# Performance work log

Hardware: AMD Instinct MI355X
Metric: run time of the kernel (lower is better)

The kernel has to match this reference:

```python
import jax, jax.numpy as jnp
import numpy as np

N, M, F_IN, F_OUT, B = 8192, 4096, 256, 128, 2048
NEG = -9e15
EPS = 1e-5


def leaky(x, slope=0.2):
    return jnp.where(x > 0, x, slope * x)


def batchnorm(x, gamma, beta):
    # BatchNorm1d training-mode semantics: biased batch stats over dim 0
    m = x.mean(axis=0)
    v = jnp.var(x, axis=0)
    return (x - m) * jax.lax.rsqrt(v + EPS) * gamma + beta


def setup_inputs() -> dict:
    key = jax.random.key(0)
    ks = jax.random.split(key, 12)
    inp = {}
    inp["Sinput"] = jax.random.normal(ks[0], (N, F_IN), dtype=jnp.float32)
    inp["Rinput"] = jax.random.normal(ks[1], (M, F_IN), dtype=jnp.float32)
    inp["inter_adj"] = jax.random.randint(ks[2], (N, M), 0, 2).astype(jnp.int32)
    inp["city_adj"] = jax.random.randint(ks[3], (N, N), 0, 2).astype(jnp.int32)
    inp["province_adj"] = jax.random.randint(ks[4], (N, N), 0, 2).astype(jnp.int32)
    inp["source_index"] = jax.random.randint(ks[5], (B,), 0, N).astype(jnp.int32)
    s_w = 1.414 * np.sqrt(6.0 / (F_IN + F_OUT))  # xavier_uniform gain=1.414
    s_a = 1.414 * np.sqrt(6.0 / (2 * F_OUT + 1))
    inp["W1"] = jax.random.uniform(ks[6], (F_IN, F_OUT), jnp.float32, -s_w, s_w)
    inp["W2"] = jax.random.uniform(ks[7], (F_IN, F_OUT), jnp.float32, -s_w, s_w)
    inp["a"] = jax.random.uniform(ks[8], (2 * F_OUT, 1), jnp.float32, -s_a, s_a)
    inp["a3"] = jax.random.uniform(ks[9], (2 * F_OUT, 1), jnp.float32, -s_a, s_a)
    inp["a4"] = jax.random.uniform(ks[10], (2 * F_OUT, 1), jnp.float32, -s_a, s_a)
    inp["bn1_gamma"] = jnp.ones((F_OUT,), jnp.float32)
    inp["bn1_beta"] = jnp.zeros((F_OUT,), jnp.float32)
    inp["bn2_gamma"] = jnp.ones((F_OUT,), jnp.float32)
    inp["bn2_beta"] = jnp.zeros((F_OUT,), jnp.float32)
    return inp


def reference(Sinput, Rinput, inter_adj, city_adj, province_adj, source_index,
              W1, W2, a, a3, a4, bn1_gamma, bn1_beta, bn2_gamma, bn2_beta):
    F = W1.shape[1]
    h1 = Rinput @ W1            # [M, F]
    h2 = Sinput @ W2            # [N, F]
    # Decomposed GAT score: cat([h1[m], h2[n]]) @ a == h1[m]@a[:F] + h2[n]@a[F:]
    e12 = leaky((h2 @ a[F:, 0])[:, None] + (h1 @ a[:F, 0])[None, :])  # [N, M]
    att_inter = jax.nn.softmax(jnp.where(inter_adj > 0, e12, NEG), axis=1)
    h2_ = h2[source_index]      # [B, F]
    # cat([h2_, h2_]) @ a3 -> h2_ @ (a3[:F] + a3[F:]), constant along N axis
    s3 = leaky(h2_ @ (a3[:F, 0] + a3[F:, 0]))  # [B]
    s4 = leaky(h2_ @ (a4[:F, 0] + a4[F:, 0]))  # [B]
    Nn = Sinput.shape[0]
    e3 = jnp.broadcast_to(s3[:, None], (s3.shape[0], Nn))
    e4 = jnp.broadcast_to(s4[:, None], (s4.shape[0], Nn))
    att3 = jax.nn.softmax(jnp.where(city_adj[source_index] > 0, e3, NEG), axis=1)
    att4 = jax.nn.softmax(jnp.where(province_adj[source_index] > 0, e4, NEG), axis=1)
    InterRC = att_inter @ h1                    # [N, F]
    IntraNC = att3.T @ h2_ + att4.T @ h2_       # [N, F]
    v_output = leaky(batchnorm(att_inter.T @ h2, bn1_gamma, bn1_beta))  # [M, F]
    u_output = leaky(batchnorm(InterRC + IntraNC, bn2_gamma, bn2_beta))  # [N, F]
    h_prime = u_output @ v_output.T             # [N, M]
    return jax.nn.elu(h_prime)
```

## Files before the change

kernel.cpp:

```cpp
#include <hip/hip_runtime.h>
#include <stdint.h>

#define N_ 8192
#define M_ 4096
#define FIN_ 256
#define F_ 128
#define B_ 2048

typedef __attribute__((ext_vector_type(8))) short vs8;
typedef __attribute__((ext_vector_type(8))) __bf16 vb8;
typedef __attribute__((ext_vector_type(4))) float vf4;

union ABu { vs8 s; vb8 b; };

__device__ __forceinline__ vf4 mfma16(const ABu& a, const ABu& b, vf4 c) {
    return __builtin_amdgcn_mfma_f32_16x16x32_bf16(a.b, b.b, c, 0, 0, 0);
}
__device__ __forceinline__ unsigned short f2b(float x) {
    union { float f; unsigned u; } v; v.f = x;
    unsigned r = v.u + 0x7fffu + ((v.u >> 16) & 1u);
    return (unsigned short)(r >> 16);
}
__device__ __forceinline__ float lrelu(float x) { return x > 0.f ? x : 0.2f * x; }

__device__ __forceinline__ void glds16(const unsigned short* g, void* l) {
    __builtin_amdgcn_global_load_lds((const __attribute__((address_space(1))) unsigned int*)g,
                                     (__attribute__((address_space(3))) unsigned int*)l, 16, 0, 0);
}

__global__ void k_prep(const float* __restrict__ W1, const float* __restrict__ W2,
                       unsigned short* __restrict__ W1T, unsigned short* __restrict__ W2T,
                       float4* __restrict__ Z, int nz4) {
    int id = blockIdx.x * 256 + threadIdx.x;
    if (id < 65536) {
        const float* W = (id < 32768) ? W1 : W2;
        unsigned short* WT = (id < 32768) ? W1T : W2T;
        int o = id & 32767;
        int f = o >> 8, k = o & 255;
        WT[o] = f2b(W[k * F_ + f]);
    } else {
        int z = id - 65536;
        if (z < nz4) Z[z] = make_float4(0.f, 0.f, 0.f, 0.f);
    }
}

__global__ __launch_bounds__(256) void k_hgemmF(const float* __restrict__ Rin, const float* __restrict__ Sin,
                                                const unsigned short* __restrict__ W1T,
                                                const unsigned short* __restrict__ W2T,
                                                const float* __restrict__ a,
                                                float* __restrict__ h2,
                                                unsigned short* __restrict__ h1P, unsigned short* __restrict__ h2P,
                                                float* __restrict__ s1, float* __restrict__ s2) {
    __shared__ unsigned short tb[16][136];
    __shared__ float sred[4][16];
    int t = threadIdx.x;
    int w = t >> 6, l = t & 63, lr = l & 15, lg = l >> 4;
    int gr = blockIdx.x * 16;
    const float* X; const unsigned short* WT; unsigned short* HP; float* sout; const float* av;
    int row0; bool isH2;
    if (gr < M_) { X = Rin; WT = W1T; HP = h1P; sout = s1; av = a;      row0 = gr;      isH2 = false; }
    else         { X = Sin; WT = W2T; HP = h2P; sout = s2; av = a + F_; row0 = gr - M_; isH2 = true;  }
    int fbase = w * 32;
    vf4 acc[2] = {};
    const float* xp = X + (size_t)(row0 + lr) * FIN_ + lg * 8;
#pragma unroll
    for (int kk = 0; kk < FIN_; kk += 32) {
        float4 xa = *(const float4*)(xp + kk);
        float4 xb = *(const float4*)(xp + kk + 4);
        ABu af;
        af.s[0] = (short)f2b(xa.x); af.s[1] = (short)f2b(xa.y);
        af.s[2] = (short)f2b(xa.z); af.s[3] = (short)f2b(xa.w);
        af.s[4] = (short)f2b(xb.x); af.s[5] = (short)f2b(xb.y);
        af.s[6] = (short)f2b(xb.z); af.s[7] = (short)f2b(xb.w);
#pragma unroll
        for (int q = 0; q < 2; ++q) {
            ABu bf; bf.s = *(const vs8*)(WT + (fbase + q * 16 + lr) * FIN_ + kk + lg * 8);
            acc[q] = mfma16(af, bf, acc[q]);
        }
    }
    if (isH2) {
#pragma unroll
        for (int q = 0; q < 2; ++q)
#pragma unroll
            for (int r = 0; r < 4; ++r)
                h2[(size_t)(row0 + lg * 4 + r) * F_ + fbase + q * 16 + lr] = acc[q][r];
    }
#pragma unroll
    for (int q = 0; q < 2; ++q)
#pragma unroll
        for (int r = 0; r < 4; ++r)
            tb[lg * 4 + r][fbase + q * 16 + lr] = f2b(acc[q][r]);
    float a0 = av[fbase + lr], a1 = av[fbase + 16 + lr];
    float tv[4];
#pragma unroll
    for (int r = 0; r < 4; ++r) tv[r] = acc[0][r] * a0 + acc[1][r] * a1;
#pragma unroll
    for (int off = 1; off < 16; off <<= 1)
#pragma unroll
        for (int r = 0; r < 4; ++r) tv[r] += __shfl_xor(tv[r], off, 64);
    if ((l & 15) == 0)
#pragma unroll
        for (int r = 0; r < 4; ++r) sred[w][lg * 4 + r] = tv[r];
    __syncthreads();
    {
        int f = t >> 1, half = t & 1;
        vs8 o;
#pragma unroll
        for (int j = 0; j < 8; ++j) o[j] = (short)tb[half * 8 + j][f];
        *(vs8*)(HP + ((size_t)(row0 >> 5) * 128 + f) * 32 + (row0 & 16) + half * 8) = o;
    }
    if (t < 16) {
        float s = sred[0][t] + sred[1][t] + sred[2][t] + sred[3][t];
        sout[row0 + t] = s;
    }
}

__global__ __launch_bounds__(256) void k_adjgather(const int* __restrict__ inter, const float* __restrict__ s1,
                                                   const float* __restrict__ s2, unsigned short* __restrict__ bm,
                                                   float* __restrict__ rowmax, float* __restrict__ rowinv,
                                                   const int* __restrict__ city, const int* __restrict__ prov,
                                                   const int* __restrict__ src,
                                                   uint32_t* __restrict__ BMtc, uint32_t* __restrict__ BMtp,
                                                   float* __restrict__ w3, float* __restrict__ w4,
                                                   const float* __restrict__ h2, unsigned short* __restrict__ h2wP) {
    __shared__ float wred[8];
    int t = threadIdx.x;
    int wv = t >> 6, ln = t & 63;
    if (blockIdx.x < N_) {
        int n = blockIdx.x;
        const int* rp = inter + (size_t)n * M_ + t * 16;
        float sv[16]; unsigned mask = 0;
#pragma unroll
        for (int c = 0; c < 4; ++c) {
            int4 v = *(const int4*)(rp + c * 4);
            if (v.x > 0) mask |= 1u << (c * 4 + 0);
            if (v.y > 0) mask |= 1u << (c * 4 + 1);
            if (v.z > 0) mask |= 1u << (c * 4 + 2);
            if (v.w > 0) mask |= 1u << (c * 4 + 3);
            float4 s = *(const float4*)(s1 + t * 16 + c * 4);
            sv[c * 4 + 0] = s.x; sv[c * 4 + 1] = s.y; sv[c * 4 + 2] = s.z; sv[c * 4 + 3] = s.w;
        }
        bm[(size_t)n * 256 + t] = (unsigned short)(mask & 0xffffu);
        float mx = -3.0e38f;
#pragma unroll
        for (int j = 0; j < 16; ++j) if (mask & (1u << j)) mx = fmaxf(mx, sv[j]);
        for (int off = 32; off > 0; off >>= 1) mx = fmaxf(mx, __shfl_down(mx, off, 64));
        if (ln == 0) wred[wv] = mx;
        __syncthreads();
        float s1mx = fmaxf(fmaxf(wred[0], wred[1]), fmaxf(wred[2], wred[3]));
        float s2n = s2[n];
        float rmx = lrelu(s2n + s1mx);
        float sum = 0.f;
#pragma unroll
        for (int j = 0; j < 16; ++j) if (mask & (1u << j)) sum += __expf(lrelu(s2n + sv[j]) - rmx);
        for (int off = 32; off > 0; off >>= 1) sum += __shfl_down(sum, off, 64);
        if (ln == 0) wred[4 + wv] = sum;
        __syncthreads();
        if (t == 0) {
            float tot = wred[4] + wred[5] + wred[6] + wred[7];
            bool any = s1mx > -2.9e38f;
            rowmax[n] = any ? rmx : 0.f;
            rowinv[n] = (any && tot > 0.f) ? 1.0f / tot : 0.f;
        }
    } else if (blockIdx.x < N_ + 2 * B_) {
        int bb = blockIdx.x - N_;
        int b = bb & (B_ - 1);
        bool isC = bb < B_;
        const int* adj = isC ? city : prov;
        uint32_t* BM = isC ? BMtc : BMtp;
        float* wout = isC ? w3 : w4;
        const int* rowp = adj + (size_t)src[b] * N_;
        int cnt = 0;
#pragma unroll 4
        for (int i = 0; i < N_ / 256; ++i) {
            int v = rowp[i * 256 + t];
            unsigned long long bal = __ballot(v > 0);
            cnt += (v > 0);
            if (ln == 0) {
                int widx = i * 8 + wv * 2;
                BM[(size_t)widx * B_ + b] = (uint32_t)bal;
                BM[(size_t)(widx + 1) * B_ + b] = (uint32_t)(bal >> 32);
            }
        }
        float fc = (float)cnt;
        for (int off = 32; off > 0; off >>= 1) fc += __shfl_down(fc, off, 64);
        if (ln == 0) wred[wv] = fc;
        __syncthreads();
        if (t == 0) {
            float tot = wred[0] + wred[1] + wred[2] + wred[3];
            wout[b] = tot > 0.f ? 1.0f / tot : 0.f;
        }
    } else {
        int bblk = blockIdx.x - (N_ + 2 * B_);
        int f = t & 127, halfb = t >> 7;
        vs8 o0, o1;
#pragma unroll
        for (int i = 0; i < 8; ++i) {
            int b0 = bblk * 32 + halfb * 16 + i;
            o0[i] = (short)f2b(h2[(size_t)src[b0] * F_ + f]);
            int b1 = b0 + 8;
            o1[i] = (short)f2b(h2[(size_t)src[b1] * F_ + f]);
        }
        unsigned short* dst = h2wP + ((size_t)bblk * 128 + f) * 32 + halfb * 16;
        *(vs8*)dst = o0;
        *(vs8*)(dst + 8) = o1;
    }
}

__global__ __launch_bounds__(256) void k_attmat2(const unsigned char* __restrict__ bm8,
                                                 const float* __restrict__ s1, const float* __restrict__ s2,
                                                 const float* __restrict__ rowmax, const float* __restrict__ rowinv,
                                                 unsigned short* __restrict__ attP,
                                                 unsigned short* __restrict__ attT) {
    __shared__ unsigned short tile[64][33];
    int bx = blockIdx.x;
    int mt = bx & 63, nt = bx >> 6;
    int nb = nt * 32, mb = mt * 64;
    int t = threadIdx.x;
    int mo = t & 7, nl = t >> 3;
    int n = nb + nl;
    int m = mb + mo * 8;
    unsigned bits = bm8[(size_t)n * 512 + (m >> 3)];
    float s2n = s2[n], rmx = rowmax[n], rin = rowinv[n];
    float4 sa = *(const float4*)(s1 + m);
    float4 sb = *(const float4*)(s1 + m + 4);
    float sv[8] = {sa.x, sa.y, sa.z, sa.w, sb.x, sb.y, sb.z, sb.w};
    vs8 o;
#pragma unroll
    for (int j = 0; j < 8; ++j) {
        float v = (bits & (1u << j)) ? __expf(lrelu(s2n + sv[j]) - rmx) * rin : 0.f;
        o[j] = (short)f2b(v);
        tile[mo * 8 + j][nl] = (unsigned short)o[j];
    }
    *(vs8*)(attP + ((size_t)(m >> 5) * N_ + n) * 32 + (m & 31)) = o;
    __syncthreads();
    int mr = t >> 2, sg = t & 3;
    vs8 ot;
#pragma unroll
    for (int j = 0; j < 8; ++j) ot[j] = (short)tile[mr][sg * 8 + j];
    *(vs8*)(attT + ((size_t)nt * M_ + mb + mr) * 32 + sg * 8) = ot;
}

__global__ __launch_bounds__(256) void k_gemmABC(const unsigned short* __restrict__ attP,
                                                 const unsigned short* __restrict__ attT,
                                                 const unsigned short* __restrict__ h1P,
                                                 const unsigned short* __restrict__ h2P,
                                                 const uint32_t* __restrict__ BMtc, const uint32_t* __restrict__ BMtp,
                                                 const float* __restrict__ w3, const float* __restrict__ w4,
                                                 const unsigned short* __restrict__ h2wP,
                                                 float* __restrict__ uP, float* __restrict__ vP) {
    __shared__ __align__(16) unsigned short smem[24576];
    int t = threadIdx.x;
    int w = t >> 6, l = t & 63;
    int lr = l & 15, lg = l >> 4;
    int bx = blockIdx.x;
    if (bx < 1024) {
        bool isA = bx < 512;
        int i = isA ? bx : bx - 512;
        int x, y, rowsK;
        const unsigned short* Asrc; const unsigned short* Bsrc; float* Out;
        if (isA) { x = i & 127; y = i >> 7; Asrc = attP; Bsrc = h1P;
                   Out = uP + (size_t)y * N_ * F_; rowsK = N_; }
        else     { x = i & 63;  y = i >> 6; Asrc = attT; Bsrc = h2P;
                   Out = vP + (size_t)y * M_ * F_; rowsK = M_; }
        int kbase = y * 32;
        int rb0b = x * 64;
        int rh = (w & 1) * 32;
        int fb = (w >> 1) * 64;
        int ch0 = w * 6;
        auto stage = [&](int step, int curb) {
#pragma unroll
            for (int ii = 0; ii < 6; ++ii) {
                int c = ch0 + ii;
                const unsigned short* g; int loff;
                if (c < 8) {
                    int kb = c >> 2;
                    g = Asrc + (size_t)(kbase + 2 * step + kb) * rowsK * 32 + rb0b * 32
                        + (c & 3) * 512 + l * 8;
                    loff = curb * 24576 + kb * 4096 + (c & 3) * 1024;
                } else {
                    int c2 = c - 8;
                    int kb = c2 >> 3;
                    g = Bsrc + (size_t)(kbase + 2 * step + kb) * 4096 + (c2 & 7) * 512 + l * 8;
                    loff = curb * 24576 + 8192 + kb * 8192 + (c2 & 7) * 1024;
                }
                glds16(g, (char*)smem + loff);
            }
        };
        vf4 acc[2][4] = {};
        stage(0, 0);
        __syncthreads();
        int cur = 0;
        for (int step = 0; step < 16; ++step) {
            if (step < 15) stage(step + 1, cur ^ 1);
            const char* base = (const char*)smem + cur * 24576;
#pragma unroll
            for (int kb = 0; kb < 2; ++kb) {
                ABu a0, a1, b0, b1, b2, b3;
                a0.s = *(const vs8*)(base + kb * 4096 + (rh + lr) * 64 + lg * 16);
                a1.s = *(const vs8*)(base + kb * 4096 + (rh + 16 + lr) * 64 + lg * 16);
                b0.s = *(const vs8*)(base + 8192 + kb * 8192 + (fb + lr) * 64 + lg * 16);
                b1.s = *(const vs8*)(base + 8192 + kb * 8192 + (fb + 16 + lr) * 64 + lg * 16);
                b2.s = *(const vs8*)(base + 8192 + kb * 8192 + (fb + 32 + lr) * 64 + lg * 16);
                b3.s = *(const vs8*)(base + 8192 + kb * 8192 + (fb + 48 + lr) * 64 + lg * 16);
                acc[0][0] = mfma16(a0, b0, acc[0][0]);
                acc[1][0] = mfma16(a1, b0, acc[1][0]);
                acc[0][1] = mfma16(a0, b1, acc[0][1]);
                acc[1][1] = mfma16(a1, b1, acc[1][1]);
                acc[0][2] = mfma16(a0, b2, acc[0][2]);
                acc[1][2] = mfma16(a1, b2, acc[1][2]);
                acc[0][3] = mfma16(a0, b3, acc[0][3]);
                acc[1][3] = mfma16(a1, b3, acc[1][3]);
            }
            __syncthreads();
            cur ^= 1;
        }
#pragma unroll
        for (int s = 0; s < 2; ++s)
#pragma unroll
            for (int q = 0; q < 4; ++q)
#pragma unroll
                for (int r = 0; r < 4; ++r)
                    Out[(size_t)(rb0b + rh + s * 16 + lg * 4 + r) * F_ + fb + q * 16 + lr] = acc[s][q][r];
    } else {
        int i = bx - 1024;
        int xc = i & 127, yc = i >> 7;
        int nb0 = xc * 64 + (w & 1) * 32;
        int fb = (w >> 1) * 64;
        int wi = nb0 >> 5;
        const uint32_t* bc = BMtc + (size_t)wi * B_;
        const uint32_t* bp = BMtp + (size_t)wi * B_;
        vf4 acc[2][4] = {};
        int b0s = yc * (B_ / 4);
        for (int b0 = b0s; b0 < b0s + B_ / 4; b0 += 32) {
            int bb = b0 + lg * 8;
            uint4 c0 = *(const uint4*)(bc + bb);
            uint4 c1 = *(const uint4*)(bc + bb + 4);
            uint4 p0 = *(const uint4*)(bp + bb);
            uint4 p1 = *(const uint4*)(bp + bb + 4);
            float4 wa = *(const float4*)(w3 + bb);
            float4 wb = *(const float4*)(w3 + bb + 4);
            float4 wc = *(const float4*)(w4 + bb);
            float4 wd = *(const float4*)(w4 + bb + 4);
            const unsigned short* hb = h2wP + (size_t)(b0 >> 5) * 128 * 32;
            ABu bf0, bf1, bf2, bf3;
            bf0.s = *(const vs8*)(hb + (size_t)(fb + lr) * 32 + lg * 8);
            bf1.s = *(const vs8*)(hb + (size_t)(fb + 16 + lr) * 32 + lg * 8);
            bf2.s = *(const vs8*)(hb + (size_t)(fb + 32 + lr) * 32 + lg * 8);
            bf3.s = *(const vs8*)(hb + (size_t)(fb + 48 + lr) * 32 + lg * 8);
            uint32_t cw[8] = {c0.x, c0.y, c0.z, c0.w, c1.x, c1.y, c1.z, c1.w};
            uint32_t pw[8] = {p0.x, p0.y, p0.z, p0.w, p1.x, p1.y, p1.z, p1.w};
            float w3v[8] = {wa.x, wa.y, wa.z, wa.w, wb.x, wb.y, wb.z, wb.w};
            float w4v[8] = {wc.x, wc.y, wc.z, wc.w, wd.x, wd.y, wd.z, wd.w};
            ABu af0, af1;
#pragma unroll
            for (int j = 0; j < 8; ++j) {
                float v0 = (((cw[j] >> lr) & 1u) ? w3v[j] : 0.f) + (((pw[j] >> lr) & 1u) ? w4v[j] : 0.f);
                float v1 = (((cw[j] >> (16 + lr)) & 1u) ? w3v[j] : 0.f) + (((pw[j] >> (16 + lr)) & 1u) ? w4v[j] : 0.f);
                af0.s[j] = (short)f2b(v0);
                af1.s[j] = (short)f2b(v1);
            }
            acc[0][0] = mfma16(af0, bf0, acc[0][0]);
            acc[1][0] = mfma16(af1, bf0, acc[1][0]);
            acc[0][1] = mfma16(af0, bf1, acc[0][1]);
            acc[1][1] = mfma16(af1, bf1, acc[1][1]);
            acc[0][2] = mfma16(af0, bf2, acc[0][2]);
            acc[1][2] = mfma16(af1, bf2, acc[1][2]);
            acc[0][3] = mfma16(af0, bf3, acc[0][3]);
            acc[1][3] = mfma16(af1, bf3, acc[1][3]);
        }
        float* Out = uP + (size_t)(4 + yc) * N_ * F_;
#pragma unroll
        for (int s = 0; s < 2; ++s)
#pragma unroll
            for (int q = 0; q < 4; ++q)
#pragma unroll
                for (int r = 0; r < 4; ++r)
                    Out[(size_t)(nb0 + s * 16 + lg * 4 + r) * F_ + fb + q * 16 + lr] = acc[s][q][r];
    }
}

__global__ __launch_bounds__(256) void k_bnreduce(const float* __restrict__ vP, const float* __restrict__ uP,
                                                  float* __restrict__ v_in, float* __restrict__ u_in,
                                                  float* __restrict__ stats) {
    __shared__ float r1[256], r2[256];
    int bx = blockIdx.x;
    const float* P; float* O; int R, nb_; size_t stride; float* sum; float* sq;
    if (bx < 256) { P = vP; O = v_in; R = M_; nb_ = 256; stride = (size_t)M_ * F_;
                    sum = stats; sq = stats + 128; }
    else          { P = uP; O = u_in; R = N_; nb_ = 512; stride = (size_t)N_ * F_;
                    sum = stats + 256; sq = stats + 384; bx -= 256; }
    int f = threadIdx.x & 127;
    int half = threadIdx.x >> 7;
    float s = 0.f, s2v = 0.f;
    for (int r = bx * 2 + half; r < R; r += nb_ * 2) {
        float v = 0.f;
#pragma unroll
        for (int y = 0; y < 8; ++y) v += P[(size_t)y * stride + (size_t)r * F_ + f];
        O[(size_t)r * F_ + f] = v;
        s += v; s2v += v * v;
    }
    r1[threadIdx.x] = s; r2[threadIdx.x] = s2v;
    __syncthreads();
    if (half == 0) {
        atomicAdd(&sum[f], r1[f] + r1[f + 128]);
        atomicAdd(&sq[f], r2[f] + r2[f + 128]);
    }
}

__global__ __launch_bounds__(256) void k_bnapplyF(const float* __restrict__ v_in, const float* __restrict__ u_in,
                                                  const float* __restrict__ stats,
                                                  const float* __restrict__ g1, const float* __restrict__ b1,
                                                  const float* __restrict__ g2, const float* __restrict__ b2,
                                                  unsigned short* __restrict__ v_outb, unsigned short* __restrict__ u_outb) {
    __shared__ float sc[256], sh[256];
    int t = threadIdx.x;
    {
        int which = t >> 7, f = t & 127;
        const float* sum = stats + which * 256;
        const float* sq = sum + 128;
        const float* g = which ? g2 : g1;
        const float* be = which ? b2 : b1;
        float R = which ? (float)N_ : (float)M_;
        float mean = sum[f] / R;
        float var = sq[f] / R - mean * mean;
        float s = g[f] * rsqrtf(var + 1e-5f);
        sc[t] = s; sh[t] = be[f] - mean * s;
    }
    __syncthreads();
    int id4 = blockIdx.x * 256 + t;
    int idx = id4 * 4;
    int which = idx >= M_ * F_;
    int rel = which ? idx - M_ * F_ : idx;
    const float* P = which ? u_in : v_in;
    unsigned short* Q = which ? u_outb : v_outb;
    int f0 = (rel & 127) + which * 128;
    float4 p = *(const float4*)(P + rel);
    ushort4 o;
    o.x = f2b(lrelu(p.x * sc[f0 + 0] + sh[f0 + 0]));
    o.y = f2b(lrelu(p.y * sc[f0 + 1] + sh[f0 + 1]));
    o.z = f2b(lrelu(p.z * sc[f0 + 2] + sh[f0 + 2]));
    o.w = f2b(lrelu(p.w * sc[f0 + 3] + sh[f0 + 3]));
    *(ushort4*)(Q + rel) = o;
}

__global__ __launch_bounds__(256) void k_gemmD(const unsigned short* __restrict__ U,
                                               const unsigned short* __restrict__ V,
                                               float* __restrict__ out) {
    int w = threadIdx.x >> 6, l = threadIdx.x & 63;
    int lr = l & 15, lg = l >> 4;
    int nb = blockIdx.x * 64 + w * 16;
    int mb = blockIdx.y * 64;
    vf4 acc[4] = {};
#pragma unroll
    for (int k0 = 0; k0 < F_; k0 += 32) {
        ABu af; af.s = *(const vs8*)(U + (size_t)(nb + lr) * F_ + k0 + lg * 8);
#pragma unroll
        for (int q = 0; q < 4; ++q) {
            ABu bf; bf.s = *(const vs8*)(V + (size_t)(mb + q * 16 + lr) * F_ + k0 + lg * 8);
            acc[q] = mfma16(af, bf, acc[q]);
        }
    }
#pragma unroll
    for (int q = 0; q < 4; ++q)
#pragma unroll
        for (int r = 0; r < 4; ++r) {
            int row = nb + lg * 4 + r;
            int col = mb + q * 16 + lr;
            float x = acc[q][r];
            out[(size_t)row * M_ + col] = x > 0.f ? x : __expf(x) - 1.f;
        }
}

extern "C" void kernel_launch(void* const* d_in, const int* in_sizes, int n_in,
                              void* d_out, int out_size, void* d_ws, size_t ws_size,
                              hipStream_t stream) {
    const float* Sinput = (const float*)d_in[0];
    const float* Rinput = (const float*)d_in[1];
    const int* inter_adj = (const int*)d_in[2];
    const int* city_adj = (const int*)d_in[3];
    const int* prov_adj = (const int*)d_in[4];
    const int* src = (const int*)d_in[5];
    const float* W1 = (const float*)d_in[6];
    const float* W2 = (const float*)d_in[7];
    const float* a = (const float*)d_in[8];
    const float* g1 = (const float*)d_in[11];
    const float* b1 = (const float*)d_in[12];
    const float* g2 = (const float*)d_in[13];
    const float* b2 = (const float*)d_in[14];
    float* out = (float*)d_out;

    char* ws = (char*)d_ws;
    size_t o = 0;
    auto take = [&](size_t bytes) { char* p = ws + o; o += (bytes + 255) & ~(size_t)255; return p; };
    float* stats = (float*)take(512 * 4);
    size_t zero_bytes = o;
    float* u_in = (float*)take((size_t)N_ * F_ * 4);
    float* v_in = (float*)take((size_t)M_ * F_ * 4);
    float* uP = (float*)take((size_t)8 * N_ * F_ * 4);
    float* vP = (float*)take((size_t)8 * M_ * F_ * 4);
    float* h2 = (float*)take((size_t)N_ * F_ * 4);
    unsigned short* h1P = (unsigned short*)take((size_t)(M_ / 32) * 128 * 32 * 2);
    unsigned short* h2P = (unsigned short*)take((size_t)(N_ / 32) * 128 * 32 * 2);
    unsigned short* W1T = (unsigned short*)take((size_t)F_ * FIN_ * 2);
    unsigned short* W2T = (unsigned short*)take((size_t)F_ * FIN_ * 2);
    float* s1 = (float*)take(M_ * 4);
    float* s2 = (float*)take(N_ * 4);
    float* rowmax = (float*)take(N_ * 4);
    float* rowinv = (float*)take(N_ * 4);
    float* w3 = (float*)take(B_ * 4);
    float* w4 = (float*)take(B_ * 4);
    unsigned short* h2wP = (unsigned short*)take((size_t)(B_ / 32) * 128 * 32 * 2);
    unsigned short* u_outb = (unsigned short*)take((size_t)N_ * F_ * 2);
    unsigned short* v_outb = (unsigned short*)take((size_t)M_ * F_ * 2);
    uint32_t* BMtc = (uint32_t*)take((size_t)256 * B_ * 4);
    uint32_t* BMtp = (uint32_t*)take((size_t)256 * B_ * 4);
    unsigned short* bm = (unsigned short*)take((size_t)N_ * 256 * 2);
    unsigned short* attP = (unsigned short*)take((size_t)N_ * M_ * 2);
    unsigned short* attT = (unsigned short*)take((size_t)N_ * M_ * 2);
    (void)ws_size; (void)in_sizes; (void)n_in; (void)out_size;

    int nz4 = (int)(zero_bytes / 16);
    int zblocks = (nz4 + 255) / 256;
    k_prep<<<256 + zblocks, 256, 0, stream>>>(W1, W2, W1T, W2T, (float4*)d_ws, nz4);
    k_hgemmF<<<(M_ + N_) / 16, 256, 0, stream>>>(Rinput, Sinput, W1T, W2T, a, h2, h1P, h2P, s1, s2);
    k_adjgather<<<N_ + 2 * B_ + B_ / 32, 256, 0, stream>>>(inter_adj, s1, s2, bm, rowmax, rowinv,
                                                           city_adj, prov_adj, src, BMtc, BMtp, w3, w4,
                                                           h2, h2wP);
    k_attmat2<<<16384, 256, 0, stream>>>((const unsigned char*)bm, s1, s2, rowmax, rowinv, attP, attT);
    k_gemmABC<<<1536, 256, 0, stream>>>(attP, attT, h1P, h2P, BMtc, BMtp, w3, w4, h2wP, uP, vP);
    k_bnreduce<<<768, 256, 0, stream>>>(vP, uP, v_in, u_in, stats);
    k_bnapplyF<<<(M_ + N_) * F_ / 4 / 256, 256, 0, stream>>>(v_in, u_in, stats, g1, b1, g2, b2, v_outb, u_outb);
    k_gemmD<<<dim3(N_ / 64, M_ / 64), 256, 0, stream>>>(u_outb, v_outb, out);
}
```

Baseline: 327.0 us.

## Enlarge att GEMM tiles to 128x128 and rebalance split-K partial buffers

The attention GEMMs (att@h1 and att^T@h2) now use 128-row by 128-feature tiles, with each wave computing a 64x64 sub-tile (4x4 MFMA accumulators) instead of 32x64. This doubles operand reuse from shared memory and halves A-tile reloads. The att@h1 split-K changes to 8 slices of 16 steps, so the intra-city partials move to slots 8-11 and the u partial buffer grows to 12 slices. The bnreduce kernel sums 12 partials for u, which adds extra memory traffic and register pressure in exchange for fewer, larger GEMM blocks.

```diff
diff --git a/kernel.cpp b/kernel.cpp
--- a/kernel.cpp
+++ b/kernel.cpp
@@ -249,81 +249,63 @@
                                                  const float* __restrict__ w3, const float* __restrict__ w4,
                                                  const unsigned short* __restrict__ h2wP,
                                                  float* __restrict__ uP, float* __restrict__ vP) {
-    __shared__ __align__(16) unsigned short smem[24576];
+    __shared__ __align__(16) unsigned short smem[16384];
     int t = threadIdx.x;
     int w = t >> 6, l = t & 63;
     int lr = l & 15, lg = l >> 4;
     int bx = blockIdx.x;
-    if (bx < 1024) {
+    if (bx < 768) {
         bool isA = bx < 512;
         int i = isA ? bx : bx - 512;
-        int x, y, rowsK;
+        int x, y, ns, kbase, rowsK;
         const unsigned short* Asrc; const unsigned short* Bsrc; float* Out;
-        if (isA) { x = i & 127; y = i >> 7; Asrc = attP; Bsrc = h1P;
-                   Out = uP + (size_t)y * N_ * F_; rowsK = N_; }
-        else     { x = i & 63;  y = i >> 6; Asrc = attT; Bsrc = h2P;
-                   Out = vP + (size_t)y * M_ * F_; rowsK = M_; }
-        int kbase = y * 32;
-        int rb0b = x * 64;
-        int rh = (w & 1) * 32;
-        int fb = (w >> 1) * 64;
-        int ch0 = w * 6;
-        auto stage = [&](int step, int curb) {
-#pragma unroll
-            for (int ii = 0; ii < 6; ++ii) {
-                int c = ch0 + ii;
+        if (isA) { x = i & 63; y = i >> 6; ns = 16; kbase = y * 16; rowsK = N_;
+                   Asrc = attP; Bsrc = h1P; Out = uP + (size_t)y * N_ * F_; }
+        else     { x = i & 31; y = i >> 5; ns = 32; kbase = y * 32; rowsK = M_;
+                   Asrc = attT; Bsrc = h2P; Out = vP + (size_t)y * M_ * F_; }
+        int rb0 = x * 128;
+        int rq = (w >> 1) * 64;
+        int cb = (w & 1) * 64;
+        auto stage = [&](int kb, int buf) {
+#pragma unroll
+            for (int ii = 0; ii < 4; ++ii) {
+                int c = w * 4 + ii;
                 const unsigned short* g; int loff;
-                if (c < 8) {
-                    int kb = c >> 2;
-                    g = Asrc + (size_t)(kbase + 2 * step + kb) * rowsK * 32 + rb0b * 32
-                        + (c & 3) * 512 + l * 8;
-                    loff = curb * 24576 + kb * 4096 + (c & 3) * 1024;
-                } else {
-                    int c2 = c - 8;
-                    int kb = c2 >> 3;
-                    g = Bsrc + (size_t)(kbase + 2 * step + kb) * 4096 + (c2 & 7) * 512 + l * 8;
-                    loff = curb * 24576 + 8192 + kb * 8192 + (c2 & 7) * 1024;
-                }
-                glds16(g, (char*)smem + loff);
+                if (c < 8) { g = Asrc + ((size_t)kb * rowsK + rb0) * 32 + c * 512 + l * 8;
+                             loff = buf * 8192 + c * 512; }
+                else       { g = Bsrc + (size_t)kb * 4096 + (c - 8) * 512 + l * 8;
+                             loff = buf * 8192 + 4096 + (c - 8) * 512; }
+                glds16(g, smem + loff);
             }
         };
-        vf4 acc[2][4] = {};
-        stage(0, 0);
+        vf4 acc[4][4] = {};
+        stage(kbase, 0);
         __syncthreads();
         int cur = 0;
-        for (int step = 0; step < 16; ++step) {
-            if (step < 15) stage(step + 1, cur ^ 1);
-            const char* base = (const char*)smem + cur * 24576;
-#pragma unroll
-            for (int kb = 0; kb < 2; ++kb) {
-                ABu a0, a1, b0, b1, b2, b3;
-                a0.s = *(const vs8*)(base + kb * 4096 + (rh + lr) * 64 + lg * 16);
-                a1.s = *(const vs8*)(base + kb * 4096 + (rh + 16 + lr) * 64 + lg * 16);
-                b0.s = *(const vs8*)(base + 8192 + kb * 8192 + (fb + lr) * 64 + lg * 16);
-                b1.s = *(const vs8*)(base + 8192 + kb * 8192 + (fb + 16 + lr) * 64 + lg * 16);
-                b2.s = *(const vs8*)(base + 8192 + kb * 8192 + (fb + 32 + lr) * 64 + lg * 16);
-                b3.s = *(const vs8*)(base + 8192 + kb * 8192 + (fb + 48 + lr) * 64 + lg * 16);
-                acc[0][0] = mfma16(a0, b0, acc[0][0]);
-                acc[1][0] = mfma16(a1, b0, acc[1][0]);
-                acc[0][1] = mfma16(a0, b1, acc[0][1]);
-                acc[1][1] = mfma16(a1, b1, acc[1][1]);
-                acc[0][2] = mfma16(a0, b2, acc[0][2]);
-                acc[1][2] = mfma16(a1, b2, acc[1][2]);
-                acc[0][3] = mfma16(a0, b3, acc[0][3]);
-                acc[1][3] = mfma16(a1, b3, acc[1][3]);
-            }
+        for (int step = 0; step < ns; ++step) {
+            if (step + 1 < ns) stage(kbase + step + 1, cur ^ 1);
+            const unsigned short* base = smem + cur * 8192;
+            ABu a[4], b[4];
+#pragma unroll
+            for (int s = 0; s < 4; ++s) a[s].s = *(const vs8*)(base + (rq + s * 16 + lr) * 32 + lg * 8);
+#pragma unroll
+            for (int q = 0; q < 4; ++q) b[q].s = *(const vs8*)(base + 4096 + (cb + q * 16 + lr) * 32 + lg * 8);
+#pragma unroll
+            for (int s = 0; s < 4; ++s)
+#pragma unroll
+                for (int q = 0; q < 4; ++q) acc[s][q] = mfma16(a[s], b[q], acc[s][q]);
             __syncthreads();
             cur ^= 1;
         }
 #pragma unroll
-        for (int s = 0; s < 2; ++s)
+        for (int s = 0; s < 4; ++s)
 #pragma unroll
             for (int q = 0; q < 4; ++q)
 #pragma unroll
                 for (int r = 0; r < 4; ++r)
-                    Out[(size_t)(rb0b + rh + s * 16 + lg * 4 + r) * F_ + fb + q * 16 + lr] = acc[s][q][r];
+                    Out[(size_t)(rb0 + rq + s * 16 + lg * 4 + r) * F_ + cb + q * 16 + lr] = acc[s][q][r];
     } else {
-        int i = bx - 1024;
+        int i = bx - 768;
         int xc = i & 127, yc = i >> 7;
         int nb0 = xc * 64 + (w & 1) * 32;
         int fb = (w >> 1) * 64;
@@ -369,7 +351,7 @@
             acc[0][3] = mfma16(af0, bf3, acc[0][3]);
             acc[1][3] = mfma16(af1, bf3, acc[1][3]);
         }
-        float* Out = uP + (size_t)(4 + yc) * N_ * F_;
+        float* Out = uP + (size_t)(8 + yc) * N_ * F_;
 #pragma unroll
         for (int s = 0; s < 2; ++s)
 #pragma unroll
@@ -385,26 +367,40 @@
                                                   float* __restrict__ stats) {
     __shared__ float r1[256], r2[256];
     int bx = blockIdx.x;
-    const float* P; float* O; int R, nb_; size_t stride; float* sum; float* sq;
-    if (bx < 256) { P = vP; O = v_in; R = M_; nb_ = 256; stride = (size_t)M_ * F_;
-                    sum = stats; sq = stats + 128; }
-    else          { P = uP; O = u_in; R = N_; nb_ = 512; stride = (size_t)N_ * F_;
-                    sum = stats + 256; sq = stats + 384; bx -= 256; }
     int f = threadIdx.x & 127;
     int half = threadIdx.x >> 7;
     float s = 0.f, s2v = 0.f;
-    for (int r = bx * 2 + half; r < R; r += nb_ * 2) {
-        float v = 0.f;
-#pragma unroll
-        for (int y = 0; y < 8; ++y) v += P[(size_t)y * stride + (size_t)r * F_ + f];
-        O[(size_t)r * F_ + f] = v;
-        s += v; s2v += v * v;
-    }
-    r1[threadIdx.x] = s; r2[threadIdx.x] = s2v;
-    __syncthreads();
-    if (half == 0) {
-        atomicAdd(&sum[f], r1[f] + r1[f + 128]);
-        atomicAdd(&sq[f], r2[f] + r2[f + 128]);
+    if (bx < 256) {
+        size_t stride = (size_t)M_ * F_;
+        for (int r = bx * 2 + half; r < M_; r += 512) {
+            float v = 0.f;
+#pragma unroll
+            for (int y = 0; y < 8; ++y) v += vP[(size_t)y * stride + (size_t)r * F_ + f];
+            v_in[(size_t)r * F_ + f] = v;
+            s += v; s2v += v * v;
+        }
+        r1[threadIdx.x] = s; r2[threadIdx.x] = s2v;
+        __syncthreads();
+        if (half == 0) {
+            atomicAdd(&stats[f], r1[f] + r1[f + 128]);
+            atomicAdd(&stats[128 + f], r2[f] + r2[f + 128]);
+        }
+    } else {
+        int b = bx - 256;
+        size_t stride = (size_t)N_ * F_;
+        for (int r = b * 2 + half; r < N_; r += 1024) {
+            float v = 0.f;
+#pragma unroll
+            for (int y = 0; y < 12; ++y) v += uP[(size_t)y * stride + (size_t)r * F_ + f];
+            u_in[(size_t)r * F_ + f] = v;
+            s += v; s2v += v * v;
+        }
+        r1[threadIdx.x] = s; r2[threadIdx.x] = s2v;
+        __syncthreads();
+        if (half == 0) {
+            atomicAdd(&stats[256 + f], r1[f] + r1[f + 128]);
+            atomicAdd(&stats[384 + f], r2[f] + r2[f + 128]);
+        }
     }
 }
 
@@ -497,7 +493,7 @@
     size_t zero_bytes = o;
     float* u_in = (float*)take((size_t)N_ * F_ * 4);
     float* v_in = (float*)take((size_t)M_ * F_ * 4);
-    float* uP = (float*)take((size_t)8 * N_ * F_ * 4);
+    float* uP = (float*)take((size_t)12 * N_ * F_ * 4);
     float* vP = (float*)take((size_t)8 * M_ * F_ * 4);
     float* h2 = (float*)take((size_t)N_ * F_ * 4);
     unsigned short* h1P = (unsigned short*)take((size_t)(M_ / 32) * 128 * 32 * 2);
@@ -528,7 +524,7 @@
                                                            city_adj, prov_adj, src, BMtc, BMtp, w3, w4,
                                                            h2, h2wP);
     k_attmat2<<<16384, 256, 0, stream>>>((const unsigned char*)bm, s1, s2, rowmax, rowinv, attP, attT);
-    k_gemmABC<<<1536, 256, 0, stream>>>(attP, attT, h1P, h2P, BMtc, BMtp, w3, w4, h2wP, uP, vP);
+    k_gemmABC<<<1280, 256, 0, stream>>>(attP, attT, h1P, h2P, BMtc, BMtp, w3, w4, h2wP, uP, vP);
     k_bnreduce<<<768, 256, 0, stream>>>(vP, uP, v_in, u_in, stats);
     k_bnapplyF<<<(M_ + N_) * F_ / 4 / 256, 256, 0, stream>>>(v_in, u_in, stats, g1, b1, g2, b2, v_outb, u_outb);
     k_gemmD<<<dim3(N_ / 64, M_ / 64), 256, 0, stream>>>(u_outb, v_outb, out);
```

After: 330.5 us. About the same (+1.1%).
